# Kernel tuning notes

Measured on AMD Instinct MI355X. Metric: run time of the kernel, lower is better.

The kernel has to match this reference:

```python
import jax, jax.numpy as jnp
import numpy as np

NB, H = 4, 8          # blocks, heads
B, S = 2, 1024        # batch, seq
D, HID = 512, 512     # input_dim, hidden_dim (must match, see zeros_like(x) branch)
# mod computed from neurochem BEFORE _modulate_neurochem, using init values
MOD = 0.5 * 1.1 + 0.5 * 0.7 + 0.5 * 1.3 - 0.0 * 1.2  # = 1.55


def setup_inputs() -> dict:
    key = jax.random.key(0)
    ks = jax.random.split(key, 12)
    sc = 1.0 / np.sqrt(D)
    inp = {
        "x": jax.random.normal(ks[0], (B, S, D), jnp.float32),
        "Wq": jax.random.normal(ks[1], (NB, D, HID), jnp.float32) * sc,
        "bq": jax.random.normal(ks[2], (NB, HID), jnp.float32) * sc,
        "Wk": jax.random.normal(ks[3], (NB, D, HID), jnp.float32) * sc,
        "bk": jax.random.normal(ks[4], (NB, HID), jnp.float32) * sc,
        "Wv": jax.random.normal(ks[5], (NB, D, HID), jnp.float32) * sc,
        "bv": jax.random.normal(ks[6], (NB, HID), jnp.float32) * sc,
        "Wo": jax.random.normal(ks[7], (NB, HID, D), jnp.float32) * sc,
        "bo": jax.random.normal(ks[8], (NB, D), jnp.float32) * sc,
        "strength": jax.random.uniform(ks[9], (NB, H, H), jnp.float32),
        # gate = (osc_mask * spike_mask > 0.5) materialized as 0/1 floats
        "gate": (jax.random.uniform(ks[10], (NB, H)) < 0.7).astype(jnp.float32),
    }
    return inp


def reference(x, Wq, bq, Wk, bk, Wv, bv, Wo, bo, strength, gate):
    # per-block projections (shared across heads in the original loop)
    q = jnp.einsum('bsd,ndh->nbsh', x, Wq) + bq[:, None, None, :]
    k = jnp.einsum('bsd,ndh->nbsh', x, Wk) + bk[:, None, None, :]
    v = jnp.einsum('bsd,ndh->nbsh', x, Wv) + bv[:, None, None, :]
    scores = jnp.einsum('nbsh,nbth->nbst', q, k) / jnp.sqrt(jnp.float32(HID))
    # per-head scalar bias: diagonal synaptic strength, clamped
    s = jnp.clip(jnp.diagonal(strength, axis1=1, axis2=2), 0.01, 1.0)  # [NB, H]
    scaled = scores[:, None] * s[:, :, None, None, None]  # [NB, H, B, S, S]
    probs = jax.nn.softmax(scaled, axis=-1)
    # head outputs summed with the 0/1 osc*spike gate
    head_sum = jnp.einsum('nhbst,nbtd,nh->nbsd', probs, v, gate)  # [NB, B, S, HID]
    block_out = jnp.einsum('nbsd,ndo->nbso', head_sum, Wo) + bo[:, None, None, :]
    return block_out.sum(axis=0) * jnp.float32(MOD)
```

## Files before the change

kernel.cpp:

```cpp
#include <hip/hip_runtime.h>
#include <math.h>

#define NBLK   4
#define NH     8
#define BATCH  2
#define SEQ    1024
#define DIM    512
#define HIDDEN 512
#define MODF   1.55f
#define INV_SQRT_HID 0.04419417382415922f

typedef __bf16 bf16;
typedef __bf16 bf16x4 __attribute__((ext_vector_type(4)));
typedef __bf16 bf16x8 __attribute__((ext_vector_type(8)));
typedef float  floatx4 __attribute__((ext_vector_type(4)));

constexpr int BM = 128, BN = 128, BK = 32;

__device__ __forceinline__ void load16_lds(const bf16* g, bf16* l) {
    __builtin_amdgcn_global_load_lds(
        (__attribute__((address_space(1))) void*)g,
        (__attribute__((address_space(3))) void*)l, 16, 0, 0);
}

__device__ __forceinline__ void stage32(
    const bf16* __restrict__ Ab, int lda,
    const bf16* __restrict__ Bb, int ldb, int k0,
    bf16* As, bf16* Bs, int w, int l)
{
    const int s0 = 2 * w, s1 = s0 + 1;
    const int r0 = s0 * 16 + (l >> 2);
    const int r1 = s1 * 16 + (l >> 2);
    const int kc = (l & 3) * 8;
    load16_lds(Ab + (size_t)r0 * lda + k0 + kc, As + s0 * 512);
    load16_lds(Ab + (size_t)r1 * lda + k0 + kc, As + s1 * 512);
    load16_lds(Bb + (size_t)r0 * ldb + k0 + kc, Bs + s0 * 512);
    load16_lds(Bb + (size_t)r1 * ldb + k0 + kc, Bs + s1 * 512);
}

__device__ __forceinline__ void comp32(
    const bf16* As, const bf16* Bs,
    int wr, int wc, int fr, int fk, floatx4 (&acc)[4][4])
{
    bf16x8 af[4], bg[4];
#pragma unroll
    for (int i = 0; i < 4; ++i)
        af[i] = *(const bf16x8*)&As[(wr + i * 16 + fr) * BK + fk];
#pragma unroll
    for (int j = 0; j < 4; ++j)
        bg[j] = *(const bf16x8*)&Bs[(wc + j * 16 + fr) * BK + fk];
#pragma unroll
    for (int i = 0; i < 4; ++i)
#pragma unroll
        for (int j = 0; j < 4; ++j)
            acc[i][j] = __builtin_amdgcn_mfma_f32_16x16x32_bf16(
                af[i], bg[j], acc[i][j], 0, 0, 0);
}

__device__ __forceinline__ void mfma_nt4(
    const bf16* __restrict__ A, int lda,
    const bf16* __restrict__ B, int ldb,
    int K, int m0, int n0, floatx4 (&acc)[4][4])
{
    __shared__ __align__(16) bf16 As0[BM * BK];
    __shared__ __align__(16) bf16 Bs0[BN * BK];
    __shared__ __align__(16) bf16 As1[BM * BK];
    __shared__ __align__(16) bf16 Bs1[BN * BK];

    const int tid = threadIdx.x;
    const int l   = tid & 63;
    const int w   = tid >> 6;
    const int wr  = (w >> 1) * 64;
    const int wc  = (w & 1) * 64;
    const int fr  = l & 15;
    const int fk  = (l >> 4) * 8;

    const bf16* Ab = A + (size_t)m0 * lda;
    const bf16* Bb = B + (size_t)n0 * ldb;

    const int nIter = K / BK;
    stage32(Ab, lda, Bb, ldb, 0, As0, Bs0, w, l);
    for (int k = 0; k < nIter; k += 2) {
        __syncthreads();
        if (k + 1 < nIter)
            stage32(Ab, lda, Bb, ldb, (k + 1) * BK, As1, Bs1, w, l);
        comp32(As0, Bs0, wr, wc, fr, fk, acc);
        __syncthreads();
        if (k + 2 < nIter)
            stage32(Ab, lda, Bb, ldb, (k + 2) * BK, As0, Bs0, w, l);
        comp32(As1, Bs1, wr, wc, fr, fk, acc);
    }
}

__device__ __forceinline__ void stage8(
    const bf16* __restrict__ Ab, int lda,
    const bf16* __restrict__ Bb, int ldb, int k0,
    bf16* As, bf16* Bs, int w, int l)
{
    const int row = w * 16 + (l >> 2);
    const int kc  = (l & 3) * 8;
    load16_lds(Ab + (size_t)row * lda + k0 + kc, As + w * 512);
    load16_lds(Bb + (size_t)row * ldb + k0 + kc, Bs + w * 512);
}

__device__ __forceinline__ void comp8(
    const bf16* As, const bf16* Bs,
    int wr, int wc, int fr, int fk, floatx4 (&acc)[4][2])
{
    bf16x8 af[4], bg[2];
#pragma unroll
    for (int i = 0; i < 4; ++i)
        af[i] = *(const bf16x8*)&As[(wr + i * 16 + fr) * BK + fk];
#pragma unroll
    for (int j = 0; j < 2; ++j)
        bg[j] = *(const bf16x8*)&Bs[(wc + j * 16 + fr) * BK + fk];
#pragma unroll
    for (int i = 0; i < 4; ++i)
#pragma unroll
        for (int j = 0; j < 2; ++j)
            acc[i][j] = __builtin_amdgcn_mfma_f32_16x16x32_bf16(
                af[i], bg[j], acc[i][j], 0, 0, 0);
}

__device__ __forceinline__ void mfma_nt8(
    const bf16* __restrict__ A, int lda,
    const bf16* __restrict__ B, int ldb,
    int K, int m0, int n0, floatx4 (&acc)[4][2])
{
    __shared__ __align__(16) bf16 As0[BM * BK];
    __shared__ __align__(16) bf16 Bs0[BN * BK];
    __shared__ __align__(16) bf16 As1[BM * BK];
    __shared__ __align__(16) bf16 Bs1[BN * BK];

    const int tid = threadIdx.x;
    const int l   = tid & 63;
    const int w   = tid >> 6;
    const int wr  = (w >> 2) * 64;
    const int wc  = (w & 3) * 32;
    const int fr  = l & 15;
    const int fk  = (l >> 4) * 8;

    const bf16* Ab = A + (size_t)m0 * lda;
    const bf16* Bb = B + (size_t)n0 * ldb;

    const int nIter = K / BK;
    stage8(Ab, lda, Bb, ldb, 0, As0, Bs0, w, l);
    for (int k = 0; k < nIter; k += 2) {
        __syncthreads();
        if (k + 1 < nIter)
            stage8(Ab, lda, Bb, ldb, (k + 1) * BK, As1, Bs1, w, l);
        comp8(As0, Bs0, wr, wc, fr, fk, acc);
        __syncthreads();
        if (k + 2 < nIter)
            stage8(Ab, lda, Bb, ldb, (k + 2) * BK, As0, Bs0, w, l);
        comp8(As1, Bs1, wr, wc, fr, fk, acc);
    }
}

__global__ __launch_bounds__(256) void xconv_kernel(
    const float* __restrict__ x, bf16* __restrict__ xb)
{
    const int t = blockIdx.x * 256 + threadIdx.x;
    const float4 v = ((const float4*)x)[t];
    bf16x4 o = { (bf16)v.x, (bf16)v.y, (bf16)v.z, (bf16)v.w };
    *(bf16x4*)&xb[(size_t)t * 4] = o;
}

__global__ __launch_bounds__(256) void transpose_w_kernel(
    const float* __restrict__ Wq, const float* __restrict__ Wk,
    const float* __restrict__ Wv, const float* __restrict__ Wo,
    bf16* __restrict__ WqT, bf16* __restrict__ WkT,
    bf16* __restrict__ WvT, bf16* __restrict__ WoT)
{
    __shared__ float tile[32][33];
    const int z = blockIdx.z;
    const int mat = z >> 2, n = z & 3;
    const float* src; bf16* dst;
    if (mat == 0)      { src = Wq; dst = WqT; }
    else if (mat == 1) { src = Wk; dst = WkT; }
    else if (mat == 2) { src = Wv; dst = WvT; }
    else               { src = Wo; dst = WoT; }
    src += (size_t)n * 512 * 512;
    dst += (size_t)n * 512 * 512;

    const int tx = threadIdx.x & 31, ty = threadIdx.x >> 5;
    const int x0 = blockIdx.x * 32, y0 = blockIdx.y * 32;
#pragma unroll
    for (int r = 0; r < 4; ++r)
        tile[ty + r * 8][tx] = src[(size_t)(y0 + ty + r * 8) * 512 + x0 + tx];
    __syncthreads();
#pragma unroll
    for (int r = 0; r < 4; ++r)
        dst[(size_t)(x0 + ty + r * 8) * 512 + y0 + tx] = (bf16)tile[tx][ty + r * 8];
}

__global__ __launch_bounds__(256) void proj_mfma_kernel(
    const bf16* __restrict__ xb,
    const bf16* __restrict__ WqT, const bf16* __restrict__ WkT,
    const bf16* __restrict__ WvT,
    const float* __restrict__ bq, const float* __restrict__ bk,
    const float* __restrict__ bv,
    bf16* __restrict__ Qh, bf16* __restrict__ Kh, bf16* __restrict__ Vt)
{
    const int z = blockIdx.z;
    const int n = z & 3, which = z >> 2;
    const bf16* WT; const float* bias;
    if (which == 0)      { WT = WqT; bias = bq; }
    else if (which == 1) { WT = WkT; bias = bk; }
    else                 { WT = WvT; bias = bv; }
    WT   += (size_t)n * DIM * HIDDEN;
    bias += (size_t)n * HIDDEN;

    const int m0 = blockIdx.y * BM, n0 = blockIdx.x * BN;
    floatx4 acc[4][4] = {};
    mfma_nt4(xb, DIM, WT, DIM, DIM, m0, n0, acc);

    const int l = threadIdx.x & 63, w = threadIdx.x >> 6;
    const int rb = m0 + (w >> 1) * 64 + (l >> 4) * 4;
    const int cb = n0 + (w & 1) * 64 + (l & 15);

    if (which != 2) {
        bf16* C = (which ? Kh : Qh) + (size_t)n * (BATCH * SEQ) * HIDDEN;
#pragma unroll
        for (int j = 0; j < 4; ++j) {
            const int col = cb + j * 16;
            const float bc = bias[col];
#pragma unroll
            for (int i = 0; i < 4; ++i)
#pragma unroll
                for (int r = 0; r < 4; ++r)
                    C[(size_t)(rb + i * 16 + r) * HIDDEN + col] = (bf16)(acc[i][j][r] + bc);
        }
    } else {
        const int b = m0 >> 10;
        bf16* Cv = Vt + (size_t)(n * BATCH + b) * HIDDEN * SEQ;
        const int tb = rb & (SEQ - 1);
#pragma unroll
        for (int j = 0; j < 4; ++j) {
            const int col = cb + j * 16;
            const float bc = bias[col];
#pragma unroll
            for (int i = 0; i < 4; ++i) {
                bf16x4 o = { (bf16)(acc[i][j][0] + bc), (bf16)(acc[i][j][1] + bc),
                             (bf16)(acc[i][j][2] + bc), (bf16)(acc[i][j][3] + bc) };
                *(bf16x4*)&Cv[(size_t)col * SEQ + tb + i * 16] = o;
            }
        }
    }
}

__global__ __launch_bounds__(512) void scores_mfma_kernel(
    const bf16* __restrict__ Qh, const bf16* __restrict__ Kh,
    float* __restrict__ P)
{
    const int z = blockIdx.z;
    const bf16* A = Qh + (size_t)z * SEQ * HIDDEN;
    const bf16* B = Kh + (size_t)z * SEQ * HIDDEN;
    float* C = P + (size_t)z * SEQ * SEQ;

    const int m0 = blockIdx.y * BM, n0 = blockIdx.x * BN;
    floatx4 acc[4][2] = {};
    mfma_nt8(A, HIDDEN, B, HIDDEN, HIDDEN, m0, n0, acc);

    const int l = threadIdx.x & 63, w = threadIdx.x >> 6;
    const int rb = m0 + (w >> 2) * 64 + (l >> 4) * 4;
    const int cb = n0 + (w & 3) * 32 + (l & 15);
#pragma unroll
    for (int i = 0; i < 4; ++i)
#pragma unroll
        for (int j = 0; j < 2; ++j)
#pragma unroll
            for (int r = 0; r < 4; ++r)
                C[(size_t)(rb + i * 16 + r) * SEQ + cb + j * 16] =
                    acc[i][j][r] * INV_SQRT_HID;
}

__global__ __launch_bounds__(256) void softmax_combine_kernel(
    const float* __restrict__ P, bf16* __restrict__ Pb,
    const float* __restrict__ strength, const float* __restrict__ gate)
{
    const int row = blockIdx.x;
    const int n = row >> 11;
    const float* prow = P + (size_t)row * SEQ;
    const int tid = threadIdx.x;
    const int wid = tid >> 6, lane = tid & 63;

    float4 v = ((const float4*)prow)[tid];

    float m = fmaxf(fmaxf(v.x, v.y), fmaxf(v.z, v.w));
#pragma unroll
    for (int off = 32; off > 0; off >>= 1) m = fmaxf(m, __shfl_down(m, off));
    __shared__ float redm[4];
    if (lane == 0) redm[wid] = m;
    __syncthreads();
    const float M = fmaxf(fmaxf(redm[0], redm[1]), fmaxf(redm[2], redm[3]));

    float sh[NH], gh[NH];
#pragma unroll
    for (int h = 0; h < NH; ++h) {
        sh[h] = fminf(fmaxf(strength[n * NH * NH + h * NH + h], 0.01f), 1.0f);
        gh[h] = gate[n * NH + h];
    }

    const float e[4] = { v.x - M, v.y - M, v.z - M, v.w - M };
    float E[4][NH];
    float zsum[NH];
#pragma unroll
    for (int h = 0; h < NH; ++h) zsum[h] = 0.f;
#pragma unroll
    for (int i = 0; i < 4; ++i)
#pragma unroll
        for (int h = 0; h < NH; ++h) {
            const float t = __expf(sh[h] * e[i]);
            E[i][h] = t; zsum[h] += t;
        }

#pragma unroll
    for (int h = 0; h < NH; ++h)
#pragma unroll
        for (int off = 32; off > 0; off >>= 1) zsum[h] += __shfl_down(zsum[h], off);
    __shared__ float redz[4][NH];
    if (lane == 0)
#pragma unroll
        for (int h = 0; h < NH; ++h) redz[wid][h] = zsum[h];
    __syncthreads();

    float wgt[NH];
#pragma unroll
    for (int h = 0; h < NH; ++h) {
        const float Z = redz[0][h] + redz[1][h] + redz[2][h] + redz[3][h];
        wgt[h] = gh[h] / Z;
    }

    bf16x4 o;
#pragma unroll
    for (int i = 0; i < 4; ++i) {
        float s = 0.f;
#pragma unroll
        for (int h = 0; h < NH; ++h) s += wgt[h] * E[i][h];
        o[i] = (bf16)s;
    }
    *(bf16x4*)&Pb[(size_t)row * SEQ + tid * 4] = o;
}

__global__ __launch_bounds__(512) void pv_mfma_kernel(
    const bf16* __restrict__ Pb, const bf16* __restrict__ Vt,
    bf16* __restrict__ HS)
{
    const int z = blockIdx.z;
    const bf16* A = Pb + (size_t)z * SEQ * SEQ;
    const bf16* B = Vt + (size_t)z * HIDDEN * SEQ;
    bf16* C = HS + (size_t)z * SEQ * HIDDEN;

    const int m0 = blockIdx.y * BM, n0 = blockIdx.x * BN;
    floatx4 acc[4][2] = {};
    mfma_nt8(A, SEQ, B, SEQ, SEQ, m0, n0, acc);

    const int l = threadIdx.x & 63, w = threadIdx.x >> 6;
    const int rb = m0 + (w >> 2) * 64 + (l >> 4) * 4;
    const int cb = n0 + (w & 3) * 32 + (l & 15);
#pragma unroll
    for (int i = 0; i < 4; ++i)
#pragma unroll
        for (int j = 0; j < 2; ++j)
#pragma unroll
            for (int r = 0; r < 4; ++r)
                C[(size_t)(rb + i * 16 + r) * HIDDEN + cb + j * 16] =
                    (bf16)acc[i][j][r];
}

__global__ __launch_bounds__(512) void out_partial_kernel(
    const bf16* __restrict__ HS, const bf16* __restrict__ WoT,
    float* __restrict__ Opart)
{
    const int n = blockIdx.z;
    const bf16* A = HS + (size_t)n * (BATCH * SEQ) * HIDDEN;
    const bf16* B = WoT + (size_t)n * HIDDEN * DIM;
    float* C = Opart + (size_t)n * (BATCH * SEQ) * DIM;

    const int m0 = blockIdx.y * BM, n0 = blockIdx.x * BN;
    floatx4 acc[4][2] = {};
    mfma_nt8(A, HIDDEN, B, HIDDEN, HIDDEN, m0, n0, acc);

    const int l = threadIdx.x & 63, w = threadIdx.x >> 6;
    const int rb = m0 + (w >> 2) * 64 + (l >> 4) * 4;
    const int cb = n0 + (w & 3) * 32 + (l & 15);
#pragma unroll
    for (int i = 0; i < 4; ++i)
#pragma unroll
        for (int j = 0; j < 2; ++j)
#pragma unroll
            for (int r = 0; r < 4; ++r)
                C[(size_t)(rb + i * 16 + r) * DIM + cb + j * 16] = acc[i][j][r];
}

__global__ __launch_bounds__(256) void out_reduce_kernel(
    const float* __restrict__ Opart, const float* __restrict__ bo,
    float* __restrict__ out)
{
    const size_t t = (size_t)blockIdx.x * 256 + threadIdx.x;
    const int c = (int)((t * 4) & (DIM - 1));
    const size_t stride4 = (size_t)(BATCH * SEQ) * DIM / 4;

    float4 s = ((const float4*)Opart)[t];
#pragma unroll
    for (int n = 1; n < NBLK; ++n) {
        const float4 p = ((const float4*)Opart)[t + n * stride4];
        s.x += p.x; s.y += p.y; s.z += p.z; s.w += p.w;
    }
    float4 bs = make_float4(0.f, 0.f, 0.f, 0.f);
#pragma unroll
    for (int n = 0; n < NBLK; ++n) {
        const float4 b = *(const float4*)(bo + n * DIM + c);
        bs.x += b.x; bs.y += b.y; bs.z += b.z; bs.w += b.w;
    }
    ((float4*)out)[t] = make_float4((s.x + bs.x) * MODF, (s.y + bs.y) * MODF,
                                    (s.z + bs.z) * MODF, (s.w + bs.w) * MODF);
}

extern "C" void kernel_launch(void* const* d_in, const int* in_sizes, int n_in,
                              void* d_out, int out_size, void* d_ws, size_t ws_size,
                              hipStream_t stream) {
    const float* x        = (const float*)d_in[0];
    const float* Wq       = (const float*)d_in[1];
    const float* bq       = (const float*)d_in[2];
    const float* Wk       = (const float*)d_in[3];
    const float* bk       = (const float*)d_in[4];
    const float* Wv       = (const float*)d_in[5];
    const float* bv       = (const float*)d_in[6];
    const float* Wo       = (const float*)d_in[7];
    const float* bo       = (const float*)d_in[8];
    const float* strength = (const float*)d_in[9];
    const float* gate     = (const float*)d_in[10];
    float* out = (float*)d_out;

    char* ws = (char*)d_ws;
    bf16*  xb    = (bf16*)(ws);
    bf16*  WqT   = (bf16*)(ws + (2u  << 20));
    bf16*  WkT   = (bf16*)(ws + (4u  << 20));
    bf16*  WvT   = (bf16*)(ws + (6u  << 20));
    bf16*  WoT   = (bf16*)(ws + (8u  << 20));
    bf16*  Qh    = (bf16*)(ws + (10u << 20));
    bf16*  Kh    = (bf16*)(ws + (18u << 20));
    bf16*  Vt    = (bf16*)(ws + (26u << 20));
    float* Pf    = (float*)(ws + (34u << 20));
    bf16*  Pb    = (bf16*)(ws + (10u << 20));
    bf16*  HS    = (bf16*)(ws + (34u << 20));
    float* Opart = (float*)(ws + (42u << 20));

    xconv_kernel<<<dim3((BATCH * SEQ * DIM) / 1024), 256, 0, stream>>>(x, xb);
    transpose_w_kernel<<<dim3(16, 16, 16), 256, 0, stream>>>(
        Wq, Wk, Wv, Wo, WqT, WkT, WvT, WoT);

    proj_mfma_kernel<<<dim3(HIDDEN / BN, (BATCH * SEQ) / BM, 3 * NBLK), 256, 0, stream>>>(
        xb, WqT, WkT, WvT, bq, bk, bv, Qh, Kh, Vt);

    scores_mfma_kernel<<<dim3(SEQ / BN, SEQ / BM, NBLK * BATCH), 512, 0, stream>>>(
        Qh, Kh, Pf);

    softmax_combine_kernel<<<dim3(NBLK * BATCH * SEQ), 256, 0, stream>>>(
        Pf, Pb, strength, gate);

    pv_mfma_kernel<<<dim3(HIDDEN / BN, SEQ / BM, NBLK * BATCH), 512, 0, stream>>>(
        Pb, Vt, HS);

    out_partial_kernel<<<dim3(DIM / BN, (BATCH * SEQ) / BM, NBLK), 512, 0, stream>>>(
        HS, WoT, Opart);

    out_reduce_kernel<<<dim3((BATCH * SEQ) * DIM / 4 / 256), 256, 0, stream>>>(
        Opart, bo, out);
}
```

Before: 189.1 us.

## Merge prep kernels, init output in softmax, atomically accumulate block outputs

Folds the x-to-bf16 conversion into the weight-transpose launch as an extra z-slice. The softmax launch gets extra blocks that write the summed, MOD-scaled bias into the output. The per-block output GEMM then atomically adds its scaled results into that output, removing the partial-sum buffer and the separate reduce kernel. Softmax also skips exp and reduction work for heads whose gate is zero. This trades two launches and a large fp32 round trip for fp32 atomics, whose summation order is nondeterministic.

```diff
diff --git a/kernel.cpp b/kernel.cpp
--- a/kernel.cpp
+++ b/kernel.cpp
@@ -157,23 +157,28 @@
     }
 }
 
-__global__ __launch_bounds__(256) void xconv_kernel(
-    const float* __restrict__ x, bf16* __restrict__ xb)
-{
-    const int t = blockIdx.x * 256 + threadIdx.x;
-    const float4 v = ((const float4*)x)[t];
-    bf16x4 o = { (bf16)v.x, (bf16)v.y, (bf16)v.z, (bf16)v.w };
-    *(bf16x4*)&xb[(size_t)t * 4] = o;
-}
-
-__global__ __launch_bounds__(256) void transpose_w_kernel(
+__global__ __launch_bounds__(256) void prep_kernel(
+    const float* __restrict__ x,
     const float* __restrict__ Wq, const float* __restrict__ Wk,
     const float* __restrict__ Wv, const float* __restrict__ Wo,
+    bf16* __restrict__ xb,
     bf16* __restrict__ WqT, bf16* __restrict__ WkT,
     bf16* __restrict__ WvT, bf16* __restrict__ WoT)
 {
+    const int z = blockIdx.z;
+    if (z == 16) {
+        const int bid = blockIdx.y * 16 + blockIdx.x;
+        const int base = bid * 1024 + threadIdx.x;
+#pragma unroll
+        for (int i = 0; i < 4; ++i) {
+            const int idx = base + i * 256;
+            const float4 v = ((const float4*)x)[idx];
+            bf16x4 o = { (bf16)v.x, (bf16)v.y, (bf16)v.z, (bf16)v.w };
+            *(bf16x4*)&xb[(size_t)idx * 4] = o;
+        }
+        return;
+    }
     __shared__ float tile[32][33];
-    const int z = blockIdx.z;
     const int mat = z >> 2, n = z & 3;
     const float* src; bf16* dst;
     if (mat == 0)      { src = Wq; dst = WqT; }
@@ -277,9 +282,29 @@
 
 __global__ __launch_bounds__(256) void softmax_combine_kernel(
     const float* __restrict__ P, bf16* __restrict__ Pb,
-    const float* __restrict__ strength, const float* __restrict__ gate)
+    const float* __restrict__ strength, const float* __restrict__ gate,
+    const float* __restrict__ bo, float* __restrict__ out)
 {
     const int row = blockIdx.x;
+    if (row >= NBLK * BATCH * SEQ) {
+        const int b = row - NBLK * BATCH * SEQ;
+        const int base = b * 4096 + threadIdx.x * 16;
+        const int c = base & (DIM - 1);
+#pragma unroll
+        for (int q = 0; q < 4; ++q) {
+            const int cc = c + q * 4;
+            float4 bs = make_float4(0.f, 0.f, 0.f, 0.f);
+#pragma unroll
+            for (int n = 0; n < NBLK; ++n) {
+                const float4 bv4 = *(const float4*)(bo + n * DIM + cc);
+                bs.x += bv4.x; bs.y += bv4.y; bs.z += bv4.z; bs.w += bv4.w;
+            }
+            ((float4*)out)[(base >> 2) + q] =
+                make_float4(bs.x * MODF, bs.y * MODF, bs.z * MODF, bs.w * MODF);
+        }
+        return;
+    }
+
     const int n = row >> 11;
     const float* prow = P + (size_t)row * SEQ;
     const int tid = threadIdx.x;
@@ -308,26 +333,29 @@
 #pragma unroll
     for (int h = 0; h < NH; ++h) zsum[h] = 0.f;
 #pragma unroll
-    for (int i = 0; i < 4; ++i)
-#pragma unroll
-        for (int h = 0; h < NH; ++h) {
+    for (int h = 0; h < NH; ++h) {
+        if (gh[h] == 0.f) continue;
+#pragma unroll
+        for (int i = 0; i < 4; ++i) {
             const float t = __expf(sh[h] * e[i]);
             E[i][h] = t; zsum[h] += t;
         }
-
-#pragma unroll
-    for (int h = 0; h < NH; ++h)
+    }
+
+    __shared__ float redz[4][NH];
+#pragma unroll
+    for (int h = 0; h < NH; ++h) {
+        if (gh[h] == 0.f) continue;
 #pragma unroll
         for (int off = 32; off > 0; off >>= 1) zsum[h] += __shfl_down(zsum[h], off);
-    __shared__ float redz[4][NH];
-    if (lane == 0)
-#pragma unroll
-        for (int h = 0; h < NH; ++h) redz[wid][h] = zsum[h];
+        if (lane == 0) redz[wid][h] = zsum[h];
+    }
     __syncthreads();
 
     float wgt[NH];
 #pragma unroll
     for (int h = 0; h < NH; ++h) {
+        if (gh[h] == 0.f) { wgt[h] = 0.f; continue; }
         const float Z = redz[0][h] + redz[1][h] + redz[2][h] + redz[3][h];
         wgt[h] = gh[h] / Z;
     }
@@ -337,7 +365,8 @@
     for (int i = 0; i < 4; ++i) {
         float s = 0.f;
 #pragma unroll
-        for (int h = 0; h < NH; ++h) s += wgt[h] * E[i][h];
+        for (int h = 0; h < NH; ++h)
+            if (gh[h] != 0.f) s += wgt[h] * E[i][h];
         o[i] = (bf16)s;
     }
     *(bf16x4*)&Pb[(size_t)row * SEQ + tid * 4] = o;
@@ -369,14 +398,13 @@
                     (bf16)acc[i][j][r];
 }
 
-__global__ __launch_bounds__(512) void out_partial_kernel(
+__global__ __launch_bounds__(512) void out_atomic_kernel(
     const bf16* __restrict__ HS, const bf16* __restrict__ WoT,
-    float* __restrict__ Opart)
+    float* __restrict__ out)
 {
     const int n = blockIdx.z;
     const bf16* A = HS + (size_t)n * (BATCH * SEQ) * HIDDEN;
     const bf16* B = WoT + (size_t)n * HIDDEN * DIM;
-    float* C = Opart + (size_t)n * (BATCH * SEQ) * DIM;
 
     const int m0 = blockIdx.y * BM, n0 = blockIdx.x * BN;
     floatx4 acc[4][2] = {};
@@ -391,31 +419,8 @@
         for (int j = 0; j < 2; ++j)
 #pragma unroll
             for (int r = 0; r < 4; ++r)
-                C[(size_t)(rb + i * 16 + r) * DIM + cb + j * 16] = acc[i][j][r];
-}
-
-__global__ __launch_bounds__(256) void out_reduce_kernel(
-    const float* __restrict__ Opart, const float* __restrict__ bo,
-    float* __restrict__ out)
-{
-    const size_t t = (size_t)blockIdx.x * 256 + threadIdx.x;
-    const int c = (int)((t * 4) & (DIM - 1));
-    const size_t stride4 = (size_t)(BATCH * SEQ) * DIM / 4;
-
-    float4 s = ((const float4*)Opart)[t];
-#pragma unroll
-    for (int n = 1; n < NBLK; ++n) {
-        const float4 p = ((const float4*)Opart)[t + n * stride4];
-        s.x += p.x; s.y += p.y; s.z += p.z; s.w += p.w;
-    }
-    float4 bs = make_float4(0.f, 0.f, 0.f, 0.f);
-#pragma unroll
-    for (int n = 0; n < NBLK; ++n) {
-        const float4 b = *(const float4*)(bo + n * DIM + c);
-        bs.x += b.x; bs.y += b.y; bs.z += b.z; bs.w += b.w;
-    }
-    ((float4*)out)[t] = make_float4((s.x + bs.x) * MODF, (s.y + bs.y) * MODF,
-                                    (s.z + bs.z) * MODF, (s.w + bs.w) * MODF);
+                atomicAdd(&out[(size_t)(rb + i * 16 + r) * DIM + cb + j * 16],
+                          acc[i][j][r] * MODF);
 }
 
 extern "C" void kernel_launch(void* const* d_in, const int* in_sizes, int n_in,
@@ -446,11 +451,9 @@
     float* Pf    = (float*)(ws + (34u << 20));
     bf16*  Pb    = (bf16*)(ws + (10u << 20));
     bf16*  HS    = (bf16*)(ws + (34u << 20));
-    float* Opart = (float*)(ws + (42u << 20));
-
-    xconv_kernel<<<dim3((BATCH * SEQ * DIM) / 1024), 256, 0, stream>>>(x, xb);
-    transpose_w_kernel<<<dim3(16, 16, 16), 256, 0, stream>>>(
-        Wq, Wk, Wv, Wo, WqT, WkT, WvT, WoT);
+
+    prep_kernel<<<dim3(16, 16, 17), 256, 0, stream>>>(
+        x, Wq, Wk, Wv, Wo, xb, WqT, WkT, WvT, WoT);
 
     proj_mfma_kernel<<<dim3(HIDDEN / BN, (BATCH * SEQ) / BM, 3 * NBLK), 256, 0, stream>>>(
         xb, WqT, WkT, WvT, bq, bk, bv, Qh, Kh, Vt);
@@ -458,15 +461,12 @@
     scores_mfma_kernel<<<dim3(SEQ / BN, SEQ / BM, NBLK * BATCH), 512, 0, stream>>>(
         Qh, Kh, Pf);
 
-    softmax_combine_kernel<<<dim3(NBLK * BATCH * SEQ), 256, 0, stream>>>(
-        Pf, Pb, strength, gate);
+    softmax_combine_kernel<<<dim3(NBLK * BATCH * SEQ + 256), 256, 0, stream>>>(
+        Pf, Pb, strength, gate, bo, out);
 
     pv_mfma_kernel<<<dim3(HIDDEN / BN, SEQ / BM, NBLK * BATCH), 512, 0, stream>>>(
         Pb, Vt, HS);
 
-    out_partial_kernel<<<dim3(DIM / BN, (BATCH * SEQ) / BM, NBLK), 512, 0, stream>>>(
-        HS, WoT, Opart);
-
-    out_reduce_kernel<<<dim3((BATCH * SEQ) * DIM / 4 / 256), 256, 0, stream>>>(
-        Opart, bo, out);
-}
+    out_atomic_kernel<<<dim3(DIM / BN, (BATCH * SEQ) / BM, NBLK), 512, 0, stream>>>(
+        HS, WoT, out);
+}
```

Result: no change. 192.7 us (+1.9%).
